# Kernel tuning notes

Hardware: AMD Instinct MI355X
Metric: run time of the kernel (lower is better)

The kernel has to match this reference:

```python
import jax, jax.numpy as jnp
import numpy as np

N_NODES = 200000
N_EDGES = 6400000
D_FEAT = 128
N_CLASSES = 40


def setup_inputs() -> dict:
    key = jax.random.key(0)
    ks = jax.random.split(key, 10)
    s_in = 1.0 / np.sqrt(D_FEAT)
    return {
        "x": jax.random.normal(ks[0], (N_NODES, D_FEAT), dtype=jnp.float32),
        "edge_index": jax.random.randint(ks[1], (2, N_EDGES), 0, N_NODES, dtype=jnp.int64),
        "W0": jax.random.normal(ks[2], (D_FEAT, D_FEAT), dtype=jnp.float32) * s_in,
        "b0": jnp.zeros((D_FEAT,), dtype=jnp.float32),
        "W1": jax.random.normal(ks[3], (D_FEAT, D_FEAT), dtype=jnp.float32) * s_in,
        "b1": jnp.zeros((D_FEAT,), dtype=jnp.float32),
        "W2": jax.random.normal(ks[4], (D_FEAT, D_FEAT), dtype=jnp.float32) * s_in,
        "b2": jnp.zeros((D_FEAT,), dtype=jnp.float32),
        "W3": jax.random.normal(ks[5], (D_FEAT, N_CLASSES), dtype=jnp.float32) * s_in,
        "b3": jnp.zeros((N_CLASSES,), dtype=jnp.float32),
    }


def _silu(h):
    return h * jax.nn.sigmoid(h)


def reference(x, edge_index, W0, b0, W1, b1, W2, b2, W3, b3):
    # PyG ChebConv with K=1: out = Tx_0 @ weight[0] + bias, Tx_0 = x.
    # edge_index feeds the scaled-Laplacian norm, which is unused when K == 1.
    del edge_index
    h = _silu(x @ W0 + b0)            # [N, D] ChebConv + SiLU
    h = _silu(h @ W1 + b1)            # [N, D]
    h = _silu(h @ W2 + b2)            # [N, D]
    logits = h @ W3 + b3              # [N, C]
    return jax.nn.log_softmax(logits, axis=1)
```

## Files before the change

kernel.cpp:

```cpp
#include <hip/hip_runtime.h>

#define NN 200000
#define NW 12
#define NBLK 256
#define NT 12500
#define WSTRIDE (NBLK * NW)

typedef __attribute__((ext_vector_type(8))) short bf16x8;
typedef __attribute__((ext_vector_type(4))) float f32x4;
typedef __attribute__((ext_vector_type(4))) unsigned int u32x4;

static __device__ __forceinline__ short f2bf(float f) {
    unsigned u = __builtin_bit_cast(unsigned, f);
    u += 0x7fffu + ((u >> 16) & 1u);
    return (short)(u >> 16);
}

static __device__ __forceinline__ unsigned pk2(float a, float b) {
    unsigned ua = __builtin_bit_cast(unsigned, a) + 0x8000u;
    unsigned ub = __builtin_bit_cast(unsigned, b) + 0x8000u;
    return __builtin_amdgcn_perm(ub, ua, 0x07060302u);
}

static __device__ __forceinline__ int swz(int r, int k) {
    return (r << 7) + (((k >> 3) ^ (r & 15)) << 3) + (k & 7);
}

__global__ void prep_weights_k(const float* __restrict__ W0, const float* __restrict__ W1,
                               const float* __restrict__ W2, const float* __restrict__ W3,
                               short* __restrict__ wt) {
    int e = blockIdx.x * 256 + threadIdx.x;
    if (e < 49152) {
        int l = e >> 14;
        int i = e & 16383;
        int n = i >> 7, k = i & 127;
        const float* W = (l == 0) ? W0 : ((l == 1) ? W1 : W2);
        wt[e] = f2bf(W[(k << 7) + n]);
    } else if (e < 55296) {
        int i = e - 49152;
        int n = i >> 7, k = i & 127;
        wt[e] = (n < 40) ? f2bf(W3[k * 40 + n]) : (short)0;
    }
}

__global__ __launch_bounds__(768)
void mlp_fused_k(const float* __restrict__ x, const short* __restrict__ wt,
                 const float* __restrict__ b0, const float* __restrict__ b1,
                 const float* __restrict__ b2, const float* __restrict__ b3,
                 float* __restrict__ out) {
    __shared__ __align__(16) short sW[55296];
    __shared__ __align__(16) short sA[NW][2048];

    const int tid  = (int)threadIdx.x;
    const int lane = tid & 63;
    const int wv   = tid >> 6;
    const int m    = lane & 15;
    const int quad = lane >> 4;
    short* sAw = &sA[wv][0];

    {
        const u32x4* src = (const u32x4*)wt;
        #pragma unroll
        for (int i = 0; i < 9; ++i) {
            int q = tid + i * 768;
            int R = q >> 4, c = q & 15;
            *(u32x4*)&sW[(R << 7) + ((c ^ (R & 15)) << 3)] = src[q];
        }
    }
    __syncthreads();

    float bv0[8], bv1[8], bv2[8];
    #pragma unroll
    for (int ct = 0; ct < 8; ++ct) {
        bv0[ct] = b0[(ct << 4) + m];
        bv1[ct] = b1[(ct << 4) + m];
        bv2[ct] = b2[(ct << 4) + m];
    }
    const bool val2 = (m < 8);
    float b3v0 = b3[m], b3v1 = b3[16 + m], b3v2 = val2 ? b3[32 + m] : 0.f;

    f32x4 acc[8];
    auto zacc = [&]() {
        #pragma unroll
        for (int ct = 0; ct < 8; ++ct)
            #pragma unroll
            for (int r = 0; r < 4; ++r) acc[ct][r] = 0.f;
    };

    auto epilogue = [&](const float* bv) {
        #pragma unroll
        for (int ct = 0; ct < 8; ++ct)
            #pragma unroll
            for (int r = 0; r < 4; ++r) {
                float v = acc[ct][r] + bv[ct];
                float h = v * __builtin_amdgcn_rcpf(1.f + __expf(-v));
                int rl = (quad << 2) + r;
                unsigned u = __builtin_bit_cast(unsigned, h) + 0x8000u;
                sAw[swz(rl, (ct << 4) + m)] = (short)(u >> 16);
            }
    };

    auto dense = [&](int lbase) {
        zacc();
        #pragma unroll
        for (int ks = 0; ks < 4; ++ks) {
            int kk = (ks << 5) + (quad << 3);
            bf16x8 a0 = *(const bf16x8*)&sAw[swz(m, kk)];
            #pragma unroll
            for (int ct = 0; ct < 8; ++ct) {
                bf16x8 b = *(const bf16x8*)&sW[lbase + swz((ct << 4) + m, kk)];
                acc[ct] = __builtin_amdgcn_mfma_f32_16x16x32_bf16(a0, b, acc[ct], 0, 0, 0);
            }
        }
    };

    int t = (int)blockIdx.x * NW + wv;
    f32x4 xc[8];
    {
        const f32x4* p = (const f32x4*)(x + ((long)(t * 16 + m) << 7)) + quad * 2;
        #pragma unroll
        for (int ks = 0; ks < 4; ++ks) { xc[ks * 2] = p[ks * 8]; xc[ks * 2 + 1] = p[ks * 8 + 1]; }
    }

    while (true) {
        int tn = t + WSTRIDE;
        bool has = tn < NT;
        f32x4 xn[8];
        if (has) {
            const f32x4* p = (const f32x4*)(x + ((long)(tn * 16 + m) << 7)) + quad * 2;
            #pragma unroll
            for (int ks = 0; ks < 4; ++ks) { xn[ks * 2] = p[ks * 8]; xn[ks * 2 + 1] = p[ks * 8 + 1]; }
        }

        zacc();
        #pragma unroll
        for (int ks = 0; ks < 4; ++ks) {
            f32x4 va = xc[ks * 2], vb = xc[ks * 2 + 1];
            u32x4 ua;
            ua[0] = pk2(va[0], va[1]); ua[1] = pk2(va[2], va[3]);
            ua[2] = pk2(vb[0], vb[1]); ua[3] = pk2(vb[2], vb[3]);
            bf16x8 a0 = __builtin_bit_cast(bf16x8, ua);
            int kk = (ks << 5) + (quad << 3);
            #pragma unroll
            for (int ct = 0; ct < 8; ++ct) {
                bf16x8 b = *(const bf16x8*)&sW[swz((ct << 4) + m, kk)];
                acc[ct] = __builtin_amdgcn_mfma_f32_16x16x32_bf16(a0, b, acc[ct], 0, 0, 0);
            }
        }
        epilogue(bv0);
        dense(16384);
        epilogue(bv1);
        dense(32768);
        epilogue(bv2);

        f32x4 c3[3];
        #pragma unroll
        for (int ct = 0; ct < 3; ++ct)
            #pragma unroll
            for (int r = 0; r < 4; ++r) c3[ct][r] = 0.f;
        #pragma unroll
        for (int ks = 0; ks < 4; ++ks) {
            int kk = (ks << 5) + (quad << 3);
            bf16x8 a0 = *(const bf16x8*)&sAw[swz(m, kk)];
            #pragma unroll
            for (int ct = 0; ct < 3; ++ct) {
                bf16x8 b = *(const bf16x8*)&sW[49152 + swz((ct << 4) + m, kk)];
                c3[ct] = __builtin_amdgcn_mfma_f32_16x16x32_bf16(a0, b, c3[ct], 0, 0, 0);
            }
        }
        #pragma unroll
        for (int r = 0; r < 4; ++r) {
            float v0 = c3[0][r] + b3v0;
            float v1 = c3[1][r] + b3v1;
            float v2 = c3[2][r] + b3v2;
            float mx = fmaxf(v0, v1);
            mx = val2 ? fmaxf(mx, v2) : mx;
            #pragma unroll
            for (int s = 1; s < 16; s <<= 1)
                mx = fmaxf(mx, __shfl_xor(mx, s, 64));
            float sm = __expf(v0 - mx) + __expf(v1 - mx) + (val2 ? __expf(v2 - mx) : 0.f);
            #pragma unroll
            for (int s = 1; s < 16; s <<= 1)
                sm += __shfl_xor(sm, s, 64);
            float L = mx + __logf(sm);
            int grow = t * 16 + (quad << 2) + r;
            float* orow = out + (long)grow * 40;
            orow[m]      = v0 - L;
            orow[16 + m] = v1 - L;
            if (val2) orow[32 + m] = v2 - L;
        }

        if (!has) break;
        #pragma unroll
        for (int i = 0; i < 8; ++i) xc[i] = xn[i];
        t = tn;
    }
}

extern "C" void kernel_launch(void* const* d_in, const int* in_sizes, int n_in,
                              void* d_out, int out_size, void* d_ws, size_t ws_size,
                              hipStream_t stream) {
    const float* x   = (const float*)d_in[0];
    const float* W0  = (const float*)d_in[2];
    const float* bb0 = (const float*)d_in[3];
    const float* W1  = (const float*)d_in[4];
    const float* bb1 = (const float*)d_in[5];
    const float* W2  = (const float*)d_in[6];
    const float* bb2 = (const float*)d_in[7];
    const float* W3  = (const float*)d_in[8];
    const float* bb3 = (const float*)d_in[9];
    short* wt  = (short*)d_ws;
    float* out = (float*)d_out;

    hipLaunchKernelGGL(prep_weights_k, dim3(216), dim3(256), 0, stream, W0, W1, W2, W3, wt);
    hipLaunchKernelGGL(mlp_fused_k, dim3(NBLK), dim3(768), 0, stream,
                       x, wt, bb0, bb1, bb2, bb3, out);
}
```

Before: 232.0 us.

## Cut register pressure: move biases to LDS, shorten prefetch, add MFMA priority

Biases for the three hidden layers now live in shared memory and are read per epilogue instead of being held in 24 registers. The next tile's x prefetch moves from the top of the loop to just before the final layer, so the double x buffer (xc/xn) becomes a single buffer. Together these are meant to lower VGPR use so the new waves_per_eu(3,3) hint can hold. s_setprio raises wave priority around the MFMA loops. The cost is less latency hiding for the x load and extra LDS reads per epilogue.

```diff
diff --git a/kernel.cpp b/kernel.cpp
--- a/kernel.cpp
+++ b/kernel.cpp
@@ -43,13 +43,14 @@
     }
 }
 
-__global__ __launch_bounds__(768)
+__global__ __launch_bounds__(768) __attribute__((amdgpu_waves_per_eu(3, 3)))
 void mlp_fused_k(const float* __restrict__ x, const short* __restrict__ wt,
                  const float* __restrict__ b0, const float* __restrict__ b1,
                  const float* __restrict__ b2, const float* __restrict__ b3,
                  float* __restrict__ out) {
     __shared__ __align__(16) short sW[55296];
     __shared__ __align__(16) short sA[NW][2048];
+    __shared__ __align__(16) float sB[384];
 
     const int tid  = (int)threadIdx.x;
     const int lane = tid & 63;
@@ -66,18 +67,13 @@
             int R = q >> 4, c = q & 15;
             *(u32x4*)&sW[(R << 7) + ((c ^ (R & 15)) << 3)] = src[q];
         }
+        if (tid < 384)
+            sB[tid] = (tid < 128) ? b0[tid] : (tid < 256) ? b1[tid - 128] : b2[tid - 256];
     }
     __syncthreads();
 
-    float bv0[8], bv1[8], bv2[8];
-    #pragma unroll
-    for (int ct = 0; ct < 8; ++ct) {
-        bv0[ct] = b0[(ct << 4) + m];
-        bv1[ct] = b1[(ct << 4) + m];
-        bv2[ct] = b2[(ct << 4) + m];
-    }
     const bool val2 = (m < 8);
-    float b3v0 = b3[m], b3v1 = b3[16 + m], b3v2 = val2 ? b3[32 + m] : 0.f;
+    const float b3v0 = b3[m], b3v1 = b3[16 + m], b3v2 = val2 ? b3[32 + m] : 0.f;
 
     f32x4 acc[8];
     auto zacc = [&]() {
@@ -87,12 +83,15 @@
             for (int r = 0; r < 4; ++r) acc[ct][r] = 0.f;
     };
 
-    auto epilogue = [&](const float* bv) {
+    auto epilogue = [&](int lyr) {
+        float bb[8];
+        #pragma unroll
+        for (int ct = 0; ct < 8; ++ct) bb[ct] = sB[(lyr << 7) + (ct << 4) + m];
         #pragma unroll
         for (int ct = 0; ct < 8; ++ct)
             #pragma unroll
             for (int r = 0; r < 4; ++r) {
-                float v = acc[ct][r] + bv[ct];
+                float v = acc[ct][r] + bb[ct];
                 float h = v * __builtin_amdgcn_rcpf(1.f + __expf(-v));
                 int rl = (quad << 2) + r;
                 unsigned u = __builtin_bit_cast(unsigned, h) + 0x8000u;
@@ -102,6 +101,7 @@
 
     auto dense = [&](int lbase) {
         zacc();
+        __builtin_amdgcn_s_setprio(1);
         #pragma unroll
         for (int ks = 0; ks < 4; ++ks) {
             int kk = (ks << 5) + (quad << 3);
@@ -112,34 +112,33 @@
                 acc[ct] = __builtin_amdgcn_mfma_f32_16x16x32_bf16(a0, b, acc[ct], 0, 0, 0);
             }
         }
+        __builtin_amdgcn_s_setprio(0);
     };
 
     int t = (int)blockIdx.x * NW + wv;
-    f32x4 xc[8];
+    f32x4 raw[8];
     {
         const f32x4* p = (const f32x4*)(x + ((long)(t * 16 + m) << 7)) + quad * 2;
         #pragma unroll
-        for (int ks = 0; ks < 4; ++ks) { xc[ks * 2] = p[ks * 8]; xc[ks * 2 + 1] = p[ks * 8 + 1]; }
+        for (int ks = 0; ks < 4; ++ks) { raw[ks * 2] = p[ks * 8]; raw[ks * 2 + 1] = p[ks * 8 + 1]; }
     }
 
     while (true) {
-        int tn = t + WSTRIDE;
-        bool has = tn < NT;
-        f32x4 xn[8];
-        if (has) {
-            const f32x4* p = (const f32x4*)(x + ((long)(tn * 16 + m) << 7)) + quad * 2;
-            #pragma unroll
-            for (int ks = 0; ks < 4; ++ks) { xn[ks * 2] = p[ks * 8]; xn[ks * 2 + 1] = p[ks * 8 + 1]; }
-        }
-
-        zacc();
-        #pragma unroll
-        for (int ks = 0; ks < 4; ++ks) {
-            f32x4 va = xc[ks * 2], vb = xc[ks * 2 + 1];
+        u32x4 xp[4];
+        #pragma unroll
+        for (int ks = 0; ks < 4; ++ks) {
+            f32x4 va = raw[ks * 2], vb = raw[ks * 2 + 1];
             u32x4 ua;
             ua[0] = pk2(va[0], va[1]); ua[1] = pk2(va[2], va[3]);
             ua[2] = pk2(vb[0], vb[1]); ua[3] = pk2(vb[2], vb[3]);
-            bf16x8 a0 = __builtin_bit_cast(bf16x8, ua);
+            xp[ks] = ua;
+        }
+
+        zacc();
+        __builtin_amdgcn_s_setprio(1);
+        #pragma unroll
+        for (int ks = 0; ks < 4; ++ks) {
+            bf16x8 a0 = __builtin_bit_cast(bf16x8, xp[ks]);
             int kk = (ks << 5) + (quad << 3);
             #pragma unroll
             for (int ct = 0; ct < 8; ++ct) {
@@ -147,17 +146,27 @@
                 acc[ct] = __builtin_amdgcn_mfma_f32_16x16x32_bf16(a0, b, acc[ct], 0, 0, 0);
             }
         }
-        epilogue(bv0);
+        __builtin_amdgcn_s_setprio(0);
+        epilogue(0);
         dense(16384);
-        epilogue(bv1);
+        epilogue(1);
         dense(32768);
-        epilogue(bv2);
+        epilogue(2);
+
+        int tn = t + WSTRIDE;
+        bool has = tn < NT;
+        if (has) {
+            const f32x4* p = (const f32x4*)(x + ((long)(tn * 16 + m) << 7)) + quad * 2;
+            #pragma unroll
+            for (int ks = 0; ks < 4; ++ks) { raw[ks * 2] = p[ks * 8]; raw[ks * 2 + 1] = p[ks * 8 + 1]; }
+        }
 
         f32x4 c3[3];
         #pragma unroll
         for (int ct = 0; ct < 3; ++ct)
             #pragma unroll
             for (int r = 0; r < 4; ++r) c3[ct][r] = 0.f;
+        __builtin_amdgcn_s_setprio(1);
         #pragma unroll
         for (int ks = 0; ks < 4; ++ks) {
             int kk = (ks << 5) + (quad << 3);
@@ -168,6 +177,7 @@
                 c3[ct] = __builtin_amdgcn_mfma_f32_16x16x32_bf16(a0, b, c3[ct], 0, 0, 0);
             }
         }
+        __builtin_amdgcn_s_setprio(0);
         #pragma unroll
         for (int r = 0; r < 4; ++r) {
             float v0 = c3[0][r] + b3v0;
@@ -191,8 +201,6 @@
         }
 
         if (!has) break;
-        #pragma unroll
-        for (int i = 0; i < 8; ++i) xc[i] = xn[i];
         t = tn;
     }
 }
```

Measured after the change: 216.6 us. -6.6%, faster.
